# Kernel optimization log

Measured on AMD Instinct MI355X. Metric: run time of the kernel, lower is better.

Reference implementation:

```python
import jax, jax.numpy as jnp
import numpy as np

P = 16            # num_patches = 224 // 14
T = P * P         # patches per image (256)
K = 5             # top-k templates
SIM_THR = 0.05
PATCH_THR = 2.0


def _idx2loc(idx):
    # flat patch index -> (w, h) float location, matching convert_index2location
    return jnp.stack([(idx % P).astype(jnp.float32), (idx // P).astype(jnp.float32)], axis=-1)


def setup_inputs() -> dict:
    key = jax.random.key(0)
    k1, k2, k3, k4 = jax.random.split(key, 4)
    B, N, C = 8, 32, 768
    src_feats = jax.random.normal(k1, (B, N, C, P, P), dtype=jnp.float32)
    tar_feat = jax.random.normal(k2, (B, C, P, P), dtype=jnp.float32)
    src_masks = (jax.random.uniform(k3, (B, N, P, P)) > 0.3).astype(jnp.float32)
    tar_mask = (jax.random.uniform(k4, (B, P, P)) > 0.3).astype(jnp.float32)
    return {"src_feats": src_feats, "tar_feat": tar_feat,
            "src_masks": src_masks, "tar_mask": tar_mask}


def reference(src_feats, tar_feat, src_masks, tar_mask):
    B, N, C = src_feats.shape[:3]
    # masks are already at feature resolution -> interpolate is identity; flatten
    tarm = tar_mask.reshape(B, T)                                   # (B, T)
    srcm = src_masks.reshape(B, N, T)                               # (B, N, T)
    # L2-normalize features over channel dim (F.normalize)
    tf = tar_feat / jnp.clip(jnp.linalg.norm(tar_feat, axis=1, keepdims=True), 1e-12)
    tf = tf.reshape(B, C, T)                                        # (B, C, T)
    sf = src_feats / jnp.clip(jnp.linalg.norm(src_feats, axis=2, keepdims=True), 1e-12)
    sf = sf.reshape(B, N, C, T)                                     # (B, N, C, S)
    # dense cosine similarity, masked, then thresholded to 0
    sim = jnp.einsum('bct,bncs->bnts', tf, sf)                      # (B, N, T, S)
    sim = sim * srcm[:, :, None, :] * tarm[:, None, :, None]
    sim = jnp.where(sim < SIM_THR, 0.0, sim)
    # dual nearest-neighbor search ('tar2src' direction)
    score_t2s = sim.max(axis=3)                                     # (B, N, T)
    idx_t2s = sim.argmax(axis=3).astype(jnp.int32)
    score_s2t = sim.max(axis=2)                                     # (B, N, S)
    idx_s2t = sim.argmax(axis=2).astype(jnp.int32)
    mask_sim = score_t2s >= SIM_THR
    # cycle consistency: tar -> src -> tar
    idx_s2s = jnp.take_along_axis(idx_s2t, idx_t2s, axis=2)         # (B, N, T)
    dist = jnp.linalg.norm(_idx2loc(idx_s2s) - _idx2loc(jnp.arange(T))[None, None], axis=-1)
    sim_s2s = jnp.take_along_axis(score_s2t, idx_t2s, axis=2)
    mask_cycle = (dist <= PATCH_THR) & (sim_s2s >= SIM_THR)
    # non-zero / in-mask filtering
    mask_t2s = jnp.take_along_axis(srcm, idx_t2s, axis=2)           # (B, N, T)
    mask_nz = tarm[:, None, :] * mask_t2s * (idx_s2t != 0) * (idx_t2s != 0)
    mask_all = (mask_sim & mask_cycle) * mask_nz                    # (B, N, T) float
    match_counts = mask_all.sum(axis=2)                             # (B, N)
    sim_avg = jnp.where(match_counts > 0,
                        (score_t2s * mask_all).sum(axis=2) / float(T), 0.0)
    # top-k template selection
    score_src, id_src = jax.lax.top_k(sim_avg, K)                   # (B, K)
    sel = lambda a: jnp.take_along_axis(a, id_src[:, :, None], axis=1)
    pred_mask = sel(mask_all)                                       # (B, K, T)
    score_pts = sel(score_t2s)                                      # (B, K, T)
    src_loc = _idx2loc(sel(idx_t2s)).astype(jnp.int32)              # (B, K, T, 2)
    # format_prediction: -1 outside mask, (w, h) coords inside
    grid = _idx2loc(jnp.arange(T)).astype(jnp.int32)                # (T, 2)
    nz = (pred_mask != 0)[..., None]
    tar_pts = jnp.where(nz, grid[None, None], -1)                   # (B, K, T, 2)
    src_pts = jnp.where(nz, src_loc, -1)                            # (B, K, T, 2)
    return id_src, score_src, score_pts, tar_pts, src_pts, match_counts
```

## Files before the change

### kernel.cpp

```cpp
#include <hip/hip_runtime.h>

#define T_PATCH 256
#define C_DIM   768
#define NCH     48
#define N_B     8
#define N_N     32

typedef unsigned short u16;
typedef u16   u16x8  __attribute__((ext_vector_type(8)));
typedef short s16x8  __attribute__((ext_vector_type(8)));
typedef float f32x16 __attribute__((ext_vector_type(16)));

__device__ __forceinline__ unsigned rne16(unsigned u) {
    return (u + 0x7fffu + ((u >> 16) & 1u)) >> 16;
}

__device__ __forceinline__ void split3(float x, u16& o0, u16& o1, u16& o2) {
    unsigned u0 = rne16(__float_as_uint(x));
    float f0 = __uint_as_float(u0 << 16);
    float r1 = x - f0;
    unsigned u1 = rne16(__float_as_uint(r1));
    float f1 = __uint_as_float(u1 << 16);
    float r2 = r1 - f1;
    o0 = (u16)u0; o1 = (u16)u1; o2 = (u16)(__float_as_uint(r2) >> 16);
}

__global__ void tar_split_kernel(const float* __restrict__ tar,
                                 u16* __restrict__ tS0, u16* __restrict__ tS1,
                                 u16* __restrict__ tS2, float* __restrict__ partT) {
    int blk = blockIdx.x;
    int b = blk / NCH, c = blk - b * NCH;
    int tid = threadIdx.x;
    int g = tid >> 8, t = tid & 255;
    const float* tb = tar + (size_t)b * C_DIM * T_PATCH;
    float ss = 0.f;
    u16x8 v0, v1, v2;
    #pragma unroll
    for (int j = 0; j < 8; ++j) {
        float x = tb[(c * 16 + g * 8 + j) * T_PATCH + t];
        u16 a, bb, cc;
        split3(x, a, bb, cc);
        v0[j] = a; v1[j] = bb; v2[j] = cc;
        ss = fmaf(x, x, ss);
    }
    size_t off = ((size_t)blk * 512 + tid) * 8;
    *(u16x8*)(tS0 + off) = v0;
    *(u16x8*)(tS1 + off) = v1;
    *(u16x8*)(tS2 + off) = v2;
    __shared__ float sq[512];
    sq[tid] = ss;
    __syncthreads();
    if (tid < 256) partT[blk * 256 + tid] = sq[tid] + sq[tid + 256];
}

__global__ void invt_kernel(const float* __restrict__ partT,
                            const float* __restrict__ tar_mask,
                            float* __restrict__ w_invT) {
    int b = blockIdx.x, t = threadIdx.x;
    float s = 0.f;
    for (int c = 0; c < NCH; ++c) s += partT[(b * NCH + c) * 256 + t];
    float tm = tar_mask[b * 256 + t];
    w_invT[b * 256 + t] = (tm != 0.f) ? 1.f / fmaxf(sqrtf(s), 1e-12f) : 0.f;
}

__launch_bounds__(512, 4)
__global__ void sim_kernel(const float* __restrict__ src_feats,
                           const u16* __restrict__ tS0, const u16* __restrict__ tS1,
                           const u16* __restrict__ tS2,
                           const float* __restrict__ w_invT,
                           const float* __restrict__ src_masks,
                           float* __restrict__ w_rowv, int* __restrict__ w_rowi,
                           float* __restrict__ w_s2tv, int* __restrict__ w_s2ti) {
    __shared__ __align__(16) u16 A0[2][256][8], A1[2][256][8], A2[2][256][8];
    __shared__ __align__(16) u16 B0[2][128][8], B1[2][128][8], B2[2][128][8];
    __shared__ float sqS[2][128];
    __shared__ float rowv[2][256]; __shared__ int rowi[2][256];
    __shared__ float colv[4][128]; __shared__ int coli[4][128];
    __shared__ float invT[256], invS[128];

    int bh = blockIdx.x;
    int bn = bh >> 1, half = bh & 1;
    int b  = bn >> 5;
    int tid = threadIdx.x;
    int lane = tid & 63, w = tid >> 6;
    int wm = w >> 1, wn = w & 1;
    int h = lane >> 5, l5 = lane & 31;
    int colB = tid & 127, gB = (tid >> 7) & 1;

    const float* sb = src_feats + (size_t)bn * C_DIM * T_PATCH + half * 128;

    if (tid < 256) invT[tid] = w_invT[b * 256 + tid];

    f32x16 acc[2][2];
    #pragma unroll
    for (int i = 0; i < 2; ++i)
        #pragma unroll
        for (int j = 0; j < 2; ++j) acc[i][j] = (f32x16)0.0f;

    float sss = 0.f;

    for (int c = 0; c < NCH; ++c) {
        float yv[8];
        if (tid < 256) {
            #pragma unroll
            for (int j = 0; j < 8; ++j)
                yv[j] = sb[(c * 16 + gB * 8 + j) * T_PATCH + colB];
        }
        size_t aoff = (((size_t)(b * NCH + c)) * 512 + tid) * 8;
        u16x8 a0v = *(const u16x8*)(tS0 + aoff);
        u16x8 a1v = *(const u16x8*)(tS1 + aoff);
        u16x8 a2v = *(const u16x8*)(tS2 + aoff);
        __syncthreads();
        ((u16x8*)A0)[tid] = a0v;
        ((u16x8*)A1)[tid] = a1v;
        ((u16x8*)A2)[tid] = a2v;
        if (tid < 256) {
            u16x8 b0v, b1v, b2v;
            #pragma unroll
            for (int j = 0; j < 8; ++j) {
                u16 a, bb, cc;
                split3(yv[j], a, bb, cc);
                b0v[j] = a; b1v[j] = bb; b2v[j] = cc;
                sss = fmaf(yv[j], yv[j], sss);
            }
            ((u16x8*)B0)[tid] = b0v;
            ((u16x8*)B1)[tid] = b1v;
            ((u16x8*)B2)[tid] = b2v;
        }
        __syncthreads();
        s16x8 a0[2], a1[2], a2[2];
        #pragma unroll
        for (int i = 0; i < 2; ++i) {
            int row = wm * 64 + i * 32 + l5;
            a0[i] = *(const s16x8*)&A0[h][row][0];
            a1[i] = *(const s16x8*)&A1[h][row][0];
            a2[i] = *(const s16x8*)&A2[h][row][0];
        }
        #pragma unroll
        for (int j = 0; j < 2; ++j) {
            int cl = wn * 64 + j * 32 + l5;
            s16x8 b0 = *(const s16x8*)&B0[h][cl][0];
            s16x8 b1 = *(const s16x8*)&B1[h][cl][0];
            s16x8 b2 = *(const s16x8*)&B2[h][cl][0];
            #pragma unroll
            for (int i = 0; i < 2; ++i) {
                acc[i][j] = __builtin_amdgcn_mfma_f32_32x32x16_bf16(a0[i], b0, acc[i][j], 0, 0, 0);
                acc[i][j] = __builtin_amdgcn_mfma_f32_32x32x16_bf16(a0[i], b1, acc[i][j], 0, 0, 0);
                acc[i][j] = __builtin_amdgcn_mfma_f32_32x32x16_bf16(a1[i], b0, acc[i][j], 0, 0, 0);
                acc[i][j] = __builtin_amdgcn_mfma_f32_32x32x16_bf16(a1[i], b1, acc[i][j], 0, 0, 0);
                acc[i][j] = __builtin_amdgcn_mfma_f32_32x32x16_bf16(a0[i], b2, acc[i][j], 0, 0, 0);
                acc[i][j] = __builtin_amdgcn_mfma_f32_32x32x16_bf16(a2[i], b0, acc[i][j], 0, 0, 0);
            }
        }
    }

    __syncthreads();
    if (tid < 256) ((float*)sqS)[tid] = sss;
    __syncthreads();
    if (tid < 128) {
        float ns = sqrtf(sqS[0][tid] + sqS[1][tid]);
        float smv = src_masks[bn * 256 + half * 128 + tid];
        invS[tid] = (smv != 0.f) ? 1.f / fmaxf(ns, 1e-12f) : 0.f;
    }
    __syncthreads();

    float isv[2]; int sgl[2];
    #pragma unroll
    for (int j = 0; j < 2; ++j) {
        isv[j] = invS[wn * 64 + j * 32 + l5];
        sgl[j] = half * 128 + wn * 64 + j * 32 + l5;
    }
    float cbv[2]; int cbi[2];
    #pragma unroll
    for (int j = 0; j < 2; ++j) { cbv[j] = -1.f; cbi[j] = 0; }

    #pragma unroll
    for (int i = 0; i < 2; ++i) {
        #pragma unroll
        for (int r = 0; r < 16; ++r) {
            int trow = wm * 64 + i * 32 + (r & 3) + 8 * (r >> 2) + 4 * h;
            float it = invT[trow];
            float v[2];
            #pragma unroll
            for (int j = 0; j < 2; ++j) {
                float x = acc[i][j][r] * it * isv[j];
                v[j] = (x >= 0.05f) ? x : 0.f;
            }
            float bv = -1.f; int bi = 0;
            #pragma unroll
            for (int j = 0; j < 2; ++j)
                if (v[j] > bv) { bv = v[j]; bi = sgl[j]; }
            #pragma unroll
            for (int off = 1; off < 32; off <<= 1) {
                float ov = __shfl_xor(bv, off, 64);
                int   oi = __shfl_xor(bi, off, 64);
                if (ov > bv || (ov == bv && oi < bi)) { bv = ov; bi = oi; }
            }
            if (l5 == 0) { rowv[wn][trow] = bv; rowi[wn][trow] = bi; }
            #pragma unroll
            for (int j = 0; j < 2; ++j)
                if (v[j] > cbv[j]) { cbv[j] = v[j]; cbi[j] = trow; }
        }
    }
    #pragma unroll
    for (int j = 0; j < 2; ++j) {
        float bv = cbv[j]; int bi = cbi[j];
        float ov = __shfl_xor(bv, 32, 64);
        int   oi = __shfl_xor(bi, 32, 64);
        if (ov > bv || (ov == bv && oi < bi)) { bv = ov; bi = oi; }
        if (h == 0) { colv[wm][wn * 64 + j * 32 + l5] = bv; coli[wm][wn * 64 + j * 32 + l5] = bi; }
    }
    __syncthreads();
    if (tid < 256) {
        float v0 = rowv[0][tid]; int i0 = rowi[0][tid];
        float v1 = rowv[1][tid]; int i1 = rowi[1][tid];
        if (v1 > v0 || (v1 == v0 && i1 < i0)) { v0 = v1; i0 = i1; }
        w_rowv[bh * 256 + tid] = v0;
        w_rowi[bh * 256 + tid] = i0;
    }
    if (tid < 128) {
        float bv = colv[0][tid]; int bi = coli[0][tid];
        #pragma unroll
        for (int q = 1; q < 4; ++q) {
            float ov = colv[q][tid]; int oi = coli[q][tid];
            if (ov > bv || (ov == bv && oi < bi)) { bv = ov; bi = oi; }
        }
        w_s2tv[bn * 256 + half * 128 + tid] = bv;
        w_s2ti[bn * 256 + half * 128 + tid] = bi;
    }
}

__global__ void combine_kernel(const float* __restrict__ w_rowv, const int* __restrict__ w_rowi,
                               const float* __restrict__ w_s2tv, const int* __restrict__ w_s2ti,
                               const float* __restrict__ src_masks, const float* __restrict__ tar_mask,
                               float* __restrict__ w_score, float* __restrict__ w_mall,
                               float* __restrict__ w_savg, int* __restrict__ w_idx,
                               float* __restrict__ out) {
    int bn = blockIdx.x; int b = bn >> 5; int t = threadIdx.x;
    __shared__ float sc_s2t[256]; __shared__ int ix_s2t[256];
    __shared__ float sm[256];
    __shared__ float red[8];
    sc_s2t[t] = w_s2tv[bn * 256 + t];
    ix_s2t[t] = w_s2ti[bn * 256 + t];
    sm[t]     = src_masks[bn * 256 + t];
    float v0 = w_rowv[(bn * 2) * 256 + t];     int i0 = w_rowi[(bn * 2) * 256 + t];
    float v1 = w_rowv[(bn * 2 + 1) * 256 + t]; int i1 = w_rowi[(bn * 2 + 1) * 256 + t];
    float st2s; int i;
    if (v1 > v0 || (v1 == v0 && i1 < i0)) { st2s = v1; i = i1; }
    else                                  { st2s = v0; i = i0; }
    float tmv = tar_mask[b * 256 + t];
    __syncthreads();

    bool msim = st2s >= 0.05f;
    int is2s = ix_s2t[i];
    int dw = (is2s & 15) - (t & 15);
    int dh = (is2s >> 4) - (t >> 4);
    bool cyc = (dw * dw + dh * dh <= 4) && (sc_s2t[i] >= 0.05f);
    float mnz = tmv * sm[i] *
                ((ix_s2t[t] != 0) ? 1.f : 0.f) *
                ((i != 0) ? 1.f : 0.f);
    float mall = (msim && cyc) ? mnz : 0.f;
    w_score[bn * 256 + t] = st2s;
    w_mall[bn * 256 + t]  = mall;
    w_idx[bn * 256 + t]   = i;

    float cnt = mall, svs = st2s * mall;
    #pragma unroll
    for (int off = 1; off < 64; off <<= 1) {
        cnt += __shfl_xor(cnt, off, 64);
        svs += __shfl_xor(svs, off, 64);
    }
    if ((t & 63) == 0) {
        red[(t >> 6) * 2]     = cnt;
        red[(t >> 6) * 2 + 1] = svs;
    }
    __syncthreads();
    if (t == 0) {
        float c = red[0] + red[2] + red[4] + red[6];
        float s = red[1] + red[3] + red[5] + red[7];
        w_savg[bn] = (c > 0.f) ? (s * (1.f / 256.f)) : 0.f;
        out[51280 + bn] = c;
    }
}

__global__ void final_kernel(const float* __restrict__ w_score,
                             const float* __restrict__ w_mall,
                             const float* __restrict__ w_savg,
                             const int*   __restrict__ w_idx,
                             float* __restrict__ out) {
    int b = blockIdx.x, tid = threadIdx.x;
    __shared__ float savg[32];
    __shared__ int   topid[5];
    __shared__ float topv[5];
    if (tid < 32) savg[tid] = w_savg[b * 32 + tid];
    __syncthreads();
    if (tid == 0) {
        unsigned used = 0;
        for (int k = 0; k < 5; ++k) {
            float bv = -1e30f; int bi = 0;
            for (int n = 0; n < 32; ++n) {
                if (!((used >> n) & 1u) && savg[n] > bv) { bv = savg[n]; bi = n; }
            }
            used |= (1u << bi);
            topid[k] = bi; topv[k] = bv;
        }
    }
    __syncthreads();
    if (tid < 5) {
        out[b * 5 + tid]      = (float)topid[tid];
        out[40 + b * 5 + tid] = topv[tid];
    }
    int t = tid;
    for (int k = 0; k < 5; ++k) {
        int bn = b * 32 + topid[k];
        float sc = w_score[bn * 256 + t];
        float ma = w_mall[bn * 256 + t];
        int   ii = w_idx[bn * 256 + t];
        int o = (b * 5 + k) * 256 + t;
        out[80 + o] = sc;
        bool nz = (ma != 0.f);
        out[10320 + 2 * o]     = nz ? (float)(t & 15)  : -1.f;
        out[10320 + 2 * o + 1] = nz ? (float)(t >> 4)  : -1.f;
        out[30800 + 2 * o]     = nz ? (float)(ii & 15) : -1.f;
        out[30800 + 2 * o + 1] = nz ? (float)(ii >> 4) : -1.f;
    }
}

extern "C" void kernel_launch(void* const* d_in, const int* in_sizes, int n_in,
                              void* d_out, int out_size, void* d_ws, size_t ws_size,
                              hipStream_t stream) {
    const float* src_feats = (const float*)d_in[0];
    const float* tar_feat  = (const float*)d_in[1];
    const float* src_masks = (const float*)d_in[2];
    const float* tar_mask  = (const float*)d_in[3];
    float* out = (float*)d_out;

    const size_t PLANE = (size_t)N_B * NCH * 512 * 8;
    u16* tS0 = (u16*)d_ws;
    u16* tS1 = tS0 + PLANE;
    u16* tS2 = tS1 + PLANE;
    float* partT  = (float*)(tS2 + PLANE);
    float* w_invT = partT + (size_t)N_B * NCH * 256;
    float* w_rowv = w_invT + 2048;
    int*   w_rowi = (int*)(w_rowv + 512 * 256);
    float* w_s2tv = (float*)(w_rowi + 512 * 256);
    int*   w_s2ti = (int*)(w_s2tv + 256 * 256);
    float* w_score = (float*)(w_s2ti + 256 * 256);
    float* w_mall  = w_score + 256 * 256;
    float* w_savg  = w_mall + 256 * 256;
    int*   w_idx   = (int*)(w_savg + 256);

    tar_split_kernel<<<N_B * NCH, 512, 0, stream>>>(tar_feat, tS0, tS1, tS2, partT);
    invt_kernel<<<N_B, 256, 0, stream>>>(partT, tar_mask, w_invT);
    sim_kernel<<<N_B * N_N * 2, 512, 0, stream>>>(src_feats, tS0, tS1, tS2, w_invT,
                                                  src_masks,
                                                  w_rowv, w_rowi, w_s2tv, w_s2ti);
    combine_kernel<<<N_B * N_N, 256, 0, stream>>>(w_rowv, w_rowi, w_s2tv, w_s2ti,
                                                  src_masks, tar_mask,
                                                  w_score, w_mall, w_savg, w_idx, out);
    final_kernel<<<N_B, 256, 0, stream>>>(w_score, w_mall, w_savg, w_idx, out);
}
```

Measured before the change: 369.8 us.

## Double-buffer source tiles, load target fragments directly, and remap blocks by batch

The A operand (pre-split target features) is now read straight from global memory into registers instead of being staged through LDS, which removes the A shared buffers. The B operand (source features) is double-buffered in LDS, so the next chunk is loaded and split during the MFMA work and only one barrier is needed per iteration. Block indices are remapped so that consecutive blocks take different batches, which spreads target-feature reads across L2, and s_setprio raises wave priority around the MFMA section. The cost is more global-load traffic for A per wave and higher register pressure from holding the prefetched values.

```diff
diff --git a/kernel.cpp b/kernel.cpp
--- a/kernel.cpp
+++ b/kernel.cpp
@@ -71,23 +71,32 @@
                            const float* __restrict__ src_masks,
                            float* __restrict__ w_rowv, int* __restrict__ w_rowi,
                            float* __restrict__ w_s2tv, int* __restrict__ w_s2ti) {
-    __shared__ __align__(16) u16 A0[2][256][8], A1[2][256][8], A2[2][256][8];
-    __shared__ __align__(16) u16 B0[2][128][8], B1[2][128][8], B2[2][128][8];
+    __shared__ __align__(16) u16 B0[2][2][128][8], B1[2][2][128][8], B2[2][2][128][8];
     __shared__ float sqS[2][128];
     __shared__ float rowv[2][256]; __shared__ int rowi[2][256];
     __shared__ float colv[4][128]; __shared__ int coli[4][128];
     __shared__ float invT[256], invS[128];
 
     int bh = blockIdx.x;
-    int bn = bh >> 1, half = bh & 1;
-    int b  = bn >> 5;
+    int b    = bh & 7;
+    int loc  = bh >> 3;
+    int n    = loc >> 1;
+    int half = loc & 1;
+    int bn   = b * N_N + n;
+    int lbh  = bn * 2 + half;
+
     int tid = threadIdx.x;
     int lane = tid & 63, w = tid >> 6;
     int wm = w >> 1, wn = w & 1;
     int h = lane >> 5, l5 = lane & 31;
     int colB = tid & 127, gB = (tid >> 7) & 1;
 
-    const float* sb = src_feats + (size_t)bn * C_DIM * T_PATCH + half * 128;
+    const float* sB = src_feats + (size_t)bn * C_DIM * T_PATCH
+                    + (size_t)gB * 8 * T_PATCH + half * 128 + colB;
+    size_t aoff = ((size_t)b * NCH) * 4096 + (size_t)(h * 256 + wm * 64 + l5) * 8;
+    const u16* pa0 = tS0 + aoff;
+    const u16* pa1 = tS1 + aoff;
+    const u16* pa2 = tS2 + aoff;
 
     if (tid < 256) invT[tid] = w_invT[b * 256 + tid];
 
@@ -99,49 +108,49 @@
 
     float sss = 0.f;
 
+    if (tid < 256) {
+        u16x8 b0v, b1v, b2v;
+        #pragma unroll
+        for (int j = 0; j < 8; ++j) {
+            float x = sB[j * T_PATCH];
+            u16 a, bb, cc;
+            split3(x, a, bb, cc);
+            b0v[j] = a; b1v[j] = bb; b2v[j] = cc;
+            sss = fmaf(x, x, sss);
+        }
+        ((u16x8*)B0[0])[tid] = b0v;
+        ((u16x8*)B1[0])[tid] = b1v;
+        ((u16x8*)B2[0])[tid] = b2v;
+    }
+    const float* psrc = sB + 4096;
+    __syncthreads();
+
     for (int c = 0; c < NCH; ++c) {
+        int p = c & 1;
+        s16x8 a0[2], a1[2], a2[2];
+        #pragma unroll
+        for (int i = 0; i < 2; ++i) {
+            a0[i] = *(const s16x8*)(pa0 + i * 256);
+            a1[i] = *(const s16x8*)(pa1 + i * 256);
+            a2[i] = *(const s16x8*)(pa2 + i * 256);
+        }
+        pa0 += 4096; pa1 += 4096; pa2 += 4096;
+
         float yv[8];
-        if (tid < 256) {
-            #pragma unroll
-            for (int j = 0; j < 8; ++j)
-                yv[j] = sb[(c * 16 + gB * 8 + j) * T_PATCH + colB];
-        }
-        size_t aoff = (((size_t)(b * NCH + c)) * 512 + tid) * 8;
-        u16x8 a0v = *(const u16x8*)(tS0 + aoff);
-        u16x8 a1v = *(const u16x8*)(tS1 + aoff);
-        u16x8 a2v = *(const u16x8*)(tS2 + aoff);
-        __syncthreads();
-        ((u16x8*)A0)[tid] = a0v;
-        ((u16x8*)A1)[tid] = a1v;
-        ((u16x8*)A2)[tid] = a2v;
-        if (tid < 256) {
-            u16x8 b0v, b1v, b2v;
-            #pragma unroll
-            for (int j = 0; j < 8; ++j) {
-                u16 a, bb, cc;
-                split3(yv[j], a, bb, cc);
-                b0v[j] = a; b1v[j] = bb; b2v[j] = cc;
-                sss = fmaf(yv[j], yv[j], sss);
-            }
-            ((u16x8*)B0)[tid] = b0v;
-            ((u16x8*)B1)[tid] = b1v;
-            ((u16x8*)B2)[tid] = b2v;
-        }
-        __syncthreads();
-        s16x8 a0[2], a1[2], a2[2];
-        #pragma unroll
-        for (int i = 0; i < 2; ++i) {
-            int row = wm * 64 + i * 32 + l5;
-            a0[i] = *(const s16x8*)&A0[h][row][0];
-            a1[i] = *(const s16x8*)&A1[h][row][0];
-            a2[i] = *(const s16x8*)&A2[h][row][0];
-        }
+        bool pf = (c < NCH - 1);
+        if (tid < 256 && pf) {
+            #pragma unroll
+            for (int j = 0; j < 8; ++j) yv[j] = psrc[j * T_PATCH];
+            psrc += 4096;
+        }
+
+        __builtin_amdgcn_s_setprio(1);
         #pragma unroll
         for (int j = 0; j < 2; ++j) {
             int cl = wn * 64 + j * 32 + l5;
-            s16x8 b0 = *(const s16x8*)&B0[h][cl][0];
-            s16x8 b1 = *(const s16x8*)&B1[h][cl][0];
-            s16x8 b2 = *(const s16x8*)&B2[h][cl][0];
+            s16x8 b0 = *(const s16x8*)&B0[p][h][cl][0];
+            s16x8 b1 = *(const s16x8*)&B1[p][h][cl][0];
+            s16x8 b2 = *(const s16x8*)&B2[p][h][cl][0];
             #pragma unroll
             for (int i = 0; i < 2; ++i) {
                 acc[i][j] = __builtin_amdgcn_mfma_f32_32x32x16_bf16(a0[i], b0, acc[i][j], 0, 0, 0);
@@ -152,9 +161,24 @@
                 acc[i][j] = __builtin_amdgcn_mfma_f32_32x32x16_bf16(a2[i], b0, acc[i][j], 0, 0, 0);
             }
         }
-    }
-
-    __syncthreads();
+        __builtin_amdgcn_s_setprio(0);
+
+        if (tid < 256 && pf) {
+            u16x8 b0v, b1v, b2v;
+            #pragma unroll
+            for (int j = 0; j < 8; ++j) {
+                u16 a, bb, cc;
+                split3(yv[j], a, bb, cc);
+                b0v[j] = a; b1v[j] = bb; b2v[j] = cc;
+                sss = fmaf(yv[j], yv[j], sss);
+            }
+            ((u16x8*)B0[p ^ 1])[tid] = b0v;
+            ((u16x8*)B1[p ^ 1])[tid] = b1v;
+            ((u16x8*)B2[p ^ 1])[tid] = b2v;
+        }
+        __syncthreads();
+    }
+
     if (tid < 256) ((float*)sqS)[tid] = sss;
     __syncthreads();
     if (tid < 128) {
@@ -215,8 +239,8 @@
         float v0 = rowv[0][tid]; int i0 = rowi[0][tid];
         float v1 = rowv[1][tid]; int i1 = rowi[1][tid];
         if (v1 > v0 || (v1 == v0 && i1 < i0)) { v0 = v1; i0 = i1; }
-        w_rowv[bh * 256 + tid] = v0;
-        w_rowi[bh * 256 + tid] = i0;
+        w_rowv[lbh * 256 + tid] = v0;
+        w_rowi[lbh * 256 + tid] = i0;
     }
     if (tid < 128) {
         float bv = colv[0][tid]; int bi = coli[0][tid];
```

Measured after the change: 391.8 us. 1.06x slower.
